# Kernel optimization log

Measured on AMD Instinct MI355X. Metric: run time of the kernel, lower is better.

Reference implementation:

```python
import jax, jax.numpy as jnp
import numpy as np

B, M, N, D, H = 8, 64, 64, 256, 8

def setup_inputs() -> dict:
    key = jax.random.key(0)
    kx, kq, kk, kv, ko = jax.random.split(key, 5)
    x = jax.random.normal(kx, (B, M, N, D), dtype=jnp.float32)
    q = jax.random.normal(kq, (H, D, D), dtype=jnp.float32)
    k = jax.random.normal(kk, (D, D), dtype=jnp.float32)
    v = jax.random.normal(kv, (D, D), dtype=jnp.float32)
    o = jax.random.normal(ko, (H, D, D), dtype=jnp.float32)
    return {"x": x, "q": q, "k": k, "v": v, "o": o}

def reference(x, q, k, v, o):
    # x: [b,m,n,d]; q,o: [h,d,d]; k,v: [d,d]
    Q = jnp.einsum('bmnd,hdk->bhmnk', x, q)      # [b,h,m,n,d]
    h_half = Q.shape[1] // 2
    Q1, Q2 = Q[:, :h_half], Q[:, h_half:]
    K = jnp.einsum('bmnd,dk->bmnk', x, k)        # [b,m,n,d]
    V = jnp.einsum('bmnd,dv->bmnv', x, v)        # [b,m,n,d]

    # Axis 1: attend along the m (row) axis for each column y
    logits1 = jnp.einsum('bhxyk,bzyk->bhyxz', Q1, K)   # [b,h/2,n,m,m]
    scores1 = jax.nn.softmax(logits1, axis=-1)
    O1 = jnp.einsum('bhyxz,bzyv->bhxyv', scores1, V)   # [b,h/2,m,n,d]

    # Axis 2: attend along the n (column) axis for each row x
    logits2 = jnp.einsum('bhxyk,bxzk->bhxyz', Q2, K)   # [b,h/2,m,n,n]
    scores2 = jax.nn.softmax(logits2, axis=-1)
    O2 = jnp.einsum('bhxyz,bxzv->bhxyv', scores2, V)   # [b,h/2,m,n,d]

    O = jnp.concatenate([O1, O2], axis=1)              # [b,h,m,n,d]
    # Faithful to original: 'bhmnd,hdv->bmnd' keeps d, sums over h and v
    Z = jnp.einsum('bhmnd,hdv->bmnd', O, o)
    return Z
```

## Files before the change

### kernel.cpp

```cpp
#include <hip/hip_runtime.h>

typedef unsigned short u16;
typedef __attribute__((ext_vector_type(8))) short short8;
typedef __attribute__((ext_vector_type(4))) float f32x4;

__device__ __forceinline__ float bf2f(u16 u){ return __uint_as_float(((unsigned)u)<<16); }
__device__ __forceinline__ u16 f2bf(float f){
  unsigned u = __float_as_uint(f);
  unsigned r = u + 0x7fffu + ((u>>16)&1u);
  return (u16)(r>>16);
}

#define MFMA16(a,b,c) __builtin_amdgcn_mfma_f32_16x16x32_bf16(a,b,c,0,0,0)

static constexpr int XS_STR  = 264;
static constexpr int PS_STR  = 72;
static constexpr int WT_STR  = 72;
static constexpr int XHI_OFF = 0;
static constexpr int XLO_OFF = 16896;
static constexpr int GT_OFF  = 33792;
static constexpr int XVT_OFF = 50688;
static constexpr int PS_OFF  = 69120;
static constexpr int SMRE_OFF= 73728;
static constexpr int SMEM_BYTES = (73728 + 512)*2;

static constexpr int MH_SMEM = 70656*2;


__global__ void prep_kernel(const float* __restrict__ k, const float* __restrict__ v,
                            const float* __restrict__ o, u16* __restrict__ khi,
                            u16* __restrict__ klo, u16* __restrict__ vT,
                            float* __restrict__ soP, float4* __restrict__ outz){
  __shared__ float Ts[64*65];
  const int blk = blockIdx.x, tid = threadIdx.x;
  if (blk < 64){
    int base = blk*1024 + tid*4;
    const float4 f4 = *(const float4*)(k + base);
    ushort4 hv, lv;
    hv.x=f2bf(f4.x); lv.x=f2bf(f4.x-bf2f(hv.x));
    hv.y=f2bf(f4.y); lv.y=f2bf(f4.y-bf2f(hv.y));
    hv.z=f2bf(f4.z); lv.z=f2bf(f4.z-bf2f(hv.z));
    hv.w=f2bf(f4.w); lv.w=f2bf(f4.w-bf2f(hv.w));
    *(ushort4*)&khi[base] = hv;
    *(ushort4*)&klo[base] = lv;
  } else if (blk < 80){
    int t = blk - 64;
    const int bi = (t>>2)<<6, bj = (t&3)<<6;
    #pragma unroll
    for (int p=0;p<4;p++){
      int idx4 = tid + (p<<8);
      int i = idx4 >> 4, c4 = (idx4 & 15) << 2;
      const float4 f4 = *(const float4*)(v + ((bi+i)<<8) + bj + c4);
      Ts[i*65+c4]=f4.x; Ts[i*65+c4+1]=f4.y; Ts[i*65+c4+2]=f4.z; Ts[i*65+c4+3]=f4.w;
    }
    __syncthreads();
    #pragma unroll
    for (int p=0;p<2;p++){
      int ch = tid + (p<<8);
      int j = ch >> 3, i8 = (ch & 7) << 3;
      short8 t8;
      #pragma unroll
      for (int e=0;e<8;e++) t8[e] = (short)f2bf(Ts[(i8+e)*65 + j]);
      *(short8*)&vT[((bj+j)<<8) + bi + i8] = t8;
    }
  } else if (blk < 336){
    int p = blk - 80;
    int h = p >> 5, base = (p & 31) << 3;
    int w = tid >> 6, l = tid & 63;
    #pragma unroll
    for (int i=0;i<2;i++){
      int row = base + w*2 + i;
      const float4 f4 = *(const float4*)(o + (((h<<8)+row)<<8) + (l<<2));
      float s = f4.x + f4.y + f4.z + f4.w;
      #pragma unroll
      for (int off=32; off>=1; off>>=1) s += __shfl_xor(s, off, 64);
      if (l==0) soP[(h<<8)+row] = s;
    }
  } else {
    int z = blk - 336;
    const float4 zf4 = {0.f,0.f,0.f,0.f};
    #pragma unroll
    for (int i=0;i<16;i++) outz[z*4096 + i*256 + tid] = zf4;
  }
}

__global__ __launch_bounds__(256,1) void mh_kernel(
    const float* __restrict__ q, const u16* __restrict__ khi,
    const u16* __restrict__ klo, u16* __restrict__ mhi, u16* __restrict__ mlo)
{
  extern __shared__ u16 sm[];
  u16* Qhi = sm;
  u16* Qlo = sm + 16896;
  u16* Chi = sm + 33792;
  u16* Clo = sm + 52224;

  const int tid = threadIdx.x;
  const int w = tid >> 6, lane = tid & 63;
  const int quad = lane >> 4, m16 = lane & 15;
  const int cw = w << 6, koq = quad << 3;
  const int h = blockIdx.x >> 2, dt = (blockIdx.x & 3) << 6;

  #pragma unroll
  for (int i=0;i<16;i++){
    int idx4 = i*256 + tid;
    int tr = idx4 >> 6, c4 = (idx4 & 63) << 2;
    const float4 xv = *(const float4*)(q + (((h<<8)+dt+tr)<<8) + c4);
    ushort4 hv, lv;
    hv.x=f2bf(xv.x); lv.x=f2bf(xv.x-bf2f(hv.x));
    hv.y=f2bf(xv.y); lv.y=f2bf(xv.y-bf2f(hv.y));
    hv.z=f2bf(xv.z); lv.z=f2bf(xv.z-bf2f(hv.z));
    hv.w=f2bf(xv.w); lv.w=f2bf(xv.w-bf2f(hv.w));
    *(ushort4*)&Qhi[tr*XS_STR + c4] = hv;
    *(ushort4*)&Qlo[tr*XS_STR + c4] = lv;
  }
  __syncthreads();

  const f32x4 zf = {0.f,0.f,0.f,0.f};
  f32x4 acc[4][4];
  #pragma unroll
  for (int r=0;r<4;r++)
    #pragma unroll
    for (int c=0;c<4;c++) acc[r][c] = zf;

  short8 Bh[2][4], Bl[2][4];
  #pragma unroll
  for (int c=0;c<4;c++){
    Bh[0][c] = *(const short8*)&khi[(cw + c*16 + m16)*256 + koq];
    Bl[0][c] = *(const short8*)&klo[(cw + c*16 + m16)*256 + koq];
  }
  #pragma unroll
  for (int kk=0;kk<8;kk++){
    const int cur = kk&1, nxt = cur^1;
    if (kk<7){
      const int ko2 = ((kk+1)<<5) + koq;
      #pragma unroll
      for (int c=0;c<4;c++){
        Bh[nxt][c] = *(const short8*)&khi[(cw + c*16 + m16)*256 + ko2];
        Bl[nxt][c] = *(const short8*)&klo[(cw + c*16 + m16)*256 + ko2];
      }
    }
    const int ko = (kk<<5) + koq;
    short8 Ah[4], Al[4];
    #pragma unroll
    for (int r=0;r<4;r++) Ah[r] = *(const short8*)&Qhi[(r*16+m16)*XS_STR + ko];
    #pragma unroll
    for (int r=0;r<4;r++) Al[r] = *(const short8*)&Qlo[(r*16+m16)*XS_STR + ko];
    #pragma unroll
    for (int r=0;r<4;r++)
      #pragma unroll
      for (int c=0;c<4;c++){
        acc[r][c] = MFMA16(Ah[r], Bh[cur][c], acc[r][c]);
        acc[r][c] = MFMA16(Ah[r], Bl[cur][c], acc[r][c]);
        acc[r][c] = MFMA16(Al[r], Bh[cur][c], acc[r][c]);
      }
  }

  #pragma unroll
  for (int r=0;r<4;r++)
    #pragma unroll
    for (int c=0;c<4;c++)
      #pragma unroll
      for (int g=0; g<4; g++){
        int drow = r*16 + quad*4 + g;
        int dp   = cw + c*16 + m16;
        float vv = acc[r][c][g];
        u16 hh = f2bf(vv);
        Chi[dp*WT_STR + drow] = hh;
        Clo[dp*WT_STR + drow] = f2bf(vv - bf2f(hh));
      }
  __syncthreads();

  #pragma unroll
  for (int p=0;p<8;p++){
    int ch = tid + (p<<8);
    int dp = ch >> 3, i8 = (ch & 7) << 3;
    *(int4*)&mhi[(((h<<8)+dp)<<8) + dt + i8] = *(const int4*)&Chi[dp*WT_STR + i8];
    *(int4*)&mlo[(((h<<8)+dp)<<8) + dt + i8] = *(const int4*)&Clo[dp*WT_STR + i8];
  }
}

__global__ __launch_bounds__(512,2) void attn_kernel(
    const float* __restrict__ x, const u16* __restrict__ mhiP,
    const u16* __restrict__ mloP, const u16* __restrict__ vT,
    const float* __restrict__ soP, float* __restrict__ out)
{
  extern __shared__ u16 sm[];
  u16* Xhi = sm + XHI_OFF;
  u16* Xlo = sm + XLO_OFF;
  u16* Gt  = sm + GT_OFF;
  u16* Xvt = sm + XVT_OFF;
  u16* Ps  = sm + PS_OFF;
  float* SMf = (float*)(sm + SMRE_OFF);

  const int tid  = threadIdx.x;
  const int w    = tid >> 6, lane = tid & 63;
  const int quad = lane >> 4, m16 = lane & 15;
  const int br   = blockIdx.x >> 9;
  const int idx  = blockIdx.x & 511;
  const int b    = idx >> 6, s = idx & 63;
  const int cw   = w << 5;
  const int rs   = (w >> 1) << 4;
  const int zh   = w & 1;
  const int koq  = quad << 3;

  auto tok = [&](int t)->int {
    int m = br ? s : t;
    int n = br ? t : s;
    return (((b<<6) + m) << 14) + (n << 8);
  };

  #pragma unroll
  for (int i=0;i<8;i++){
    int idx4 = i*512 + tid;
    int tr = idx4 >> 6, c4 = (idx4 & 63) << 2;
    const float4 xv = *(const float4*)(x + tok(tr) + c4);
    ushort4 hv, lv;
    hv.x=f2bf(xv.x); lv.x=f2bf(xv.x-bf2f(hv.x));
    hv.y=f2bf(xv.y); lv.y=f2bf(xv.y-bf2f(hv.y));
    hv.z=f2bf(xv.z); lv.z=f2bf(xv.z-bf2f(hv.z));
    hv.w=f2bf(xv.w); lv.w=f2bf(xv.w-bf2f(hv.w));
    *(ushort4*)&Xhi[tr*XS_STR + c4] = hv;
    *(ushort4*)&Xlo[tr*XS_STR + c4] = lv;
  }
  __syncthreads();

  short8 XB[16];
  #pragma unroll
  for (int kk=0;kk<8;kk++)
    #pragma unroll
    for (int c=0;c<2;c++)
      XB[kk*2+c] = *(const short8*)&Xhi[((zh<<5) + c*16 + m16)*XS_STR + (kk<<5) + koq];

  const f32x4 zf = {0.f,0.f,0.f,0.f};
  f32x4 acc[4][2];

  auto mm3 = [&](const u16* __restrict__ Whi, const u16* __restrict__ Wlo){
    #pragma unroll
    for (int r=0;r<4;r++){ acc[r][0] = zf; acc[r][1] = zf; }
    short8 Bh[2][2], Bl[2][2];
    #pragma unroll
    for (int c=0;c<2;c++){
      Bh[0][c] = *(const short8*)&Whi[(cw + c*16 + m16)*256 + koq];
      Bl[0][c] = *(const short8*)&Wlo[(cw + c*16 + m16)*256 + koq];
    }
    #pragma unroll
    for (int kk=0;kk<8;kk++){
      const int cur = kk&1, nxt = cur^1;
      if (kk<7){
        const int ko2 = ((kk+1)<<5) + koq;
        #pragma unroll
        for (int c=0;c<2;c++){
          Bh[nxt][c] = *(const short8*)&Whi[(cw + c*16 + m16)*256 + ko2];
          Bl[nxt][c] = *(const short8*)&Wlo[(cw + c*16 + m16)*256 + ko2];
        }
      }
      const int ko = (kk<<5) + koq;
      short8 Ah[4], Al[4];
      #pragma unroll
      for (int r=0;r<4;r++) Ah[r] = *(const short8*)&Xhi[(r*16+m16)*XS_STR + ko];
      #pragma unroll
      for (int r=0;r<4;r++) Al[r] = *(const short8*)&Xlo[(r*16+m16)*XS_STR + ko];
      #pragma unroll
      for (int r=0;r<4;r++)
        #pragma unroll
        for (int c=0;c<2;c++){
          acc[r][c] = MFMA16(Ah[r], Bh[cur][c], acc[r][c]);
          acc[r][c] = MFMA16(Ah[r], Bl[cur][c], acc[r][c]);
          acc[r][c] = MFMA16(Al[r], Bh[cur][c], acc[r][c]);
        }
    }
  };

  {
    #pragma unroll
    for (int r=0;r<4;r++){ acc[r][0] = zf; acc[r][1] = zf; }
    #pragma unroll
    for (int kk=0;kk<8;kk++){
      const int ko = (kk<<5) + koq;
      short8 A[4], Bf[2];
      #pragma unroll
      for (int r=0;r<4;r++) A[r]  = *(const short8*)&Xhi[(r*16+m16)*XS_STR + ko];
      #pragma unroll
      for (int c=0;c<2;c++) Bf[c] = *(const short8*)&vT[(cw + c*16 + m16)*256 + ko];
      #pragma unroll
      for (int r=0;r<4;r++)
        #pragma unroll
        for (int c=0;c<2;c++) acc[r][c] = MFMA16(A[r], Bf[c], acc[r][c]);
    }
    #pragma unroll
    for (int r=0;r<4;r++)
      #pragma unroll
      for (int c=0;c<2;c++)
        #pragma unroll
        for (int g=0; g<4; g++){
          int z  = r*16 + quad*4 + g;
          int vc = cw + c*16 + m16;
          Xvt[vc*WT_STR + z] = f2bf(acc[r][c][g]);
        }
  }

  f32x4 Z[4][2];
  #pragma unroll
  for (int r=0;r<4;r++){ Z[r][0] = zf; Z[r][1] = zf; }

  for (int h=0; h<4; h++){
    const int gh = br*4 + h;

    mm3(mhiP + gh*65536, mloP + gh*65536);
    #pragma unroll
    for (int r=0;r<4;r++)
      #pragma unroll
      for (int c=0;c<2;c++)
        #pragma unroll
        for (int g=0; g<4; g++){
          int row = r*16 + quad*4 + g;
          int col = cw + c*16 + m16;
          Gt[row*XS_STR + col] = f2bf(acc[r][c][g]);
        }
    __syncthreads();

    f32x4 L[2];
    L[0] = zf; L[1] = zf;
    #pragma unroll
    for (int kk=0;kk<8;kk++){
      const int ko = (kk<<5) + koq;
      short8 A = *(const short8*)&Gt[(rs+m16)*XS_STR + ko];
      #pragma unroll
      for (int c=0;c<2;c++){
        L[c] = MFMA16(A, XB[kk*2+c], L[c]);
        short8 Bl = *(const short8*)&Xlo[((zh<<5) + c*16 + m16)*XS_STR + ko];
        L[c] = MFMA16(A, Bl, L[c]);
      }
    }
    __syncthreads();
    #pragma unroll
    for (int r=0;r<4;r++)
      #pragma unroll
      for (int c=0;c<2;c++)
        #pragma unroll
        for (int g=0; g<4; g++){
          int row = r*16 + quad*4 + g;
          int col = cw + c*16 + m16;
          float vv = acc[r][c][g];
          u16 hh = f2bf(vv);
          Gt[row*XS_STR + col] = f2bf(vv - bf2f(hh));
        }
    __syncthreads();

    #pragma unroll
    for (int kk=0;kk<8;kk++){
      const int ko = (kk<<5) + koq;
      short8 A = *(const short8*)&Gt[(rs+m16)*XS_STR + ko];
      #pragma unroll
      for (int c=0;c<2;c++)
        L[c] = MFMA16(A, XB[kk*2+c], L[c]);
    }

    float mxl[4], sml[4];
    #pragma unroll
    for (int g=0; g<4; g++){
      float mx = fmaxf(L[0][g], L[1][g]);
      #pragma unroll
      for (int off=1; off<16; off<<=1) mx = fmaxf(mx, __shfl_xor(mx, off, 64));
      float sum = 0.f;
      #pragma unroll
      for (int c=0;c<2;c++){ float e = __expf(L[c][g]-mx); L[c][g] = e; sum += e; }
      #pragma unroll
      for (int off=1; off<16; off<<=1) sum += __shfl_xor(sum, off, 64);
      mxl[g] = mx; sml[g] = sum;
      if (m16 == 0){
        int row = rs + quad*4 + g;
        SMf[row*4 + zh*2]     = mx;
        SMf[row*4 + zh*2 + 1] = sum;
      }
    }
    __syncthreads();
    #pragma unroll
    for (int g=0; g<4; g++){
      int row = rs + quad*4 + g;
      float mxo = SMf[row*4 + (zh^1)*2];
      float smo = SMf[row*4 + (zh^1)*2 + 1];
      float M   = fmaxf(mxl[g], mxo);
      float al  = __expf(mxl[g]-M), ao = __expf(mxo-M);
      float scale = al / (sml[g]*al + smo*ao);
      #pragma unroll
      for (int c=0;c<2;c++)
        Ps[row*PS_STR + (zh<<5) + c*16 + m16] = f2bf(L[c][g]*scale);
    }
    __syncthreads();

    #pragma unroll
    for (int r=0;r<4;r++){ acc[r][0] = zf; acc[r][1] = zf; }
    #pragma unroll
    for (int kk=0;kk<2;kk++){
      const int ko = (kk<<5) + koq;
      short8 A[4], Bf[2];
      #pragma unroll
      for (int r=0;r<4;r++) A[r]  = *(const short8*)&Ps[(r*16+m16)*PS_STR + ko];
      #pragma unroll
      for (int c=0;c<2;c++) Bf[c] = *(const short8*)&Xvt[(cw + c*16 + m16)*WT_STR + ko];
      #pragma unroll
      for (int r=0;r<4;r++)
        #pragma unroll
        for (int c=0;c<2;c++) acc[r][c] = MFMA16(A[r], Bf[c], acc[r][c]);
    }
    float sc[2];
    sc[0] = soP[gh*256 + cw + m16];
    sc[1] = soP[gh*256 + cw + 16 + m16];
    #pragma unroll
    for (int r=0;r<4;r++)
      #pragma unroll
      for (int c=0;c<2;c++)
        #pragma unroll
        for (int g=0; g<4; g++) Z[r][c][g] += sc[c]*acc[r][c][g];
  }

  #pragma unroll
  for (int r=0;r<4;r++)
    #pragma unroll
    for (int c=0;c<2;c++)
      #pragma unroll
      for (int g=0; g<4; g++){
        int t   = r*16 + quad*4 + g;
        int col = cw + c*16 + m16;
        atomicAdd(&out[tok(t) + col], Z[r][c][g]);
      }
}

extern "C" void kernel_launch(void* const* d_in, const int* in_sizes, int n_in,
                              void* d_out, int out_size, void* d_ws, size_t ws_size,
                              hipStream_t stream) {
  const float* x = (const float*)d_in[0];
  const float* q = (const float*)d_in[1];
  const float* k = (const float*)d_in[2];
  const float* v = (const float*)d_in[3];
  const float* o = (const float*)d_in[4];
  u16* ws   = (u16*)d_ws;
  u16* mhi  = ws;
  u16* mlo  = ws + 524288;
  u16* khi  = ws + 1048576;
  u16* klo  = ws + 1114112;
  u16* vT   = ws + 1179648;
  float* soP = (float*)(ws + 1245184);
  float* out = (float*)d_out;

  prep_kernel<<<848, 256, 0, stream>>>(k, v, o, khi, klo, vT, soP, (float4*)d_out);
  (void)hipFuncSetAttribute(reinterpret_cast<const void*>(&mh_kernel),
                            hipFuncAttributeMaxDynamicSharedMemorySize, MH_SMEM);
  mh_kernel<<<32, 256, MH_SMEM, stream>>>(q, khi, klo, mhi, mlo);

  (void)hipFuncSetAttribute(reinterpret_cast<const void*>(&attn_kernel),
                            hipFuncAttributeMaxDynamicSharedMemorySize, SMEM_BYTES);
  attn_kernel<<<1024, 512, SMEM_BYTES, stream>>>(x, mhi, mlo, vT, soP, out);
}
```

Measured before the change: 340.2 us.

## Double attention block to 1024 threads with 2x4 warp tiling and split G hi/lo buffers

Each attention block now runs 16 waves instead of 8. Each wave owns a 32x32 output tile, so per-wave accumulator and register pressure drop. G is stored as separate hi and lo buffers written at once, which removes one barrier round and the second pass over G. The softmax is now reduced across four column quarters instead of two. The V tile is hoisted into registers, and Xvt aliases the G region to fit shared memory. Occupancy per CU may fall to one block because of the shared-memory size, and the 1024-thread launch bound may force register spills.

After: 705.6 us. +107.4%, slower.

```diff
diff --git a/kernel.cpp b/kernel.cpp
--- a/kernel.cpp
+++ b/kernel.cpp
@@ -18,11 +18,12 @@
 static constexpr int WT_STR  = 72;
 static constexpr int XHI_OFF = 0;
 static constexpr int XLO_OFF = 16896;
-static constexpr int GT_OFF  = 33792;
-static constexpr int XVT_OFF = 50688;
-static constexpr int PS_OFF  = 69120;
-static constexpr int SMRE_OFF= 73728;
-static constexpr int SMEM_BYTES = (73728 + 512)*2;
+static constexpr int GHI_OFF = 33792;
+static constexpr int GLO_OFF = 50688;
+static constexpr int XVT_OFF = 33792;
+static constexpr int PS_OFF  = 67584;
+static constexpr int SMF_OFF = 72192;
+static constexpr int SMEM_BYTES = (72192 + 1024)*2;
 
 static constexpr int MH_SMEM = 70656*2;
 
@@ -179,7 +180,7 @@
   }
 }
 
-__global__ __launch_bounds__(512,2) void attn_kernel(
+__global__ __launch_bounds__(1024,4) void attn_kernel(
     const float* __restrict__ x, const u16* __restrict__ mhiP,
     const u16* __restrict__ mloP, const u16* __restrict__ vT,
     const float* __restrict__ soP, float* __restrict__ out)
@@ -187,10 +188,11 @@
   extern __shared__ u16 sm[];
   u16* Xhi = sm + XHI_OFF;
   u16* Xlo = sm + XLO_OFF;
-  u16* Gt  = sm + GT_OFF;
+  u16* Ghi = sm + GHI_OFF;
+  u16* Glo = sm + GLO_OFF;
   u16* Xvt = sm + XVT_OFF;
+  float* SMf = (float*)(sm + SMF_OFF);
   u16* Ps  = sm + PS_OFF;
-  float* SMf = (float*)(sm + SMRE_OFF);
 
   const int tid  = threadIdx.x;
   const int w    = tid >> 6, lane = tid & 63;
@@ -198,9 +200,10 @@
   const int br   = blockIdx.x >> 9;
   const int idx  = blockIdx.x & 511;
   const int b    = idx >> 6, s = idx & 63;
-  const int cw   = w << 5;
-  const int rs   = (w >> 1) << 4;
-  const int zh   = w & 1;
+  const int rb   = (w >> 3) << 5;
+  const int cb   = (w & 7) << 5;
+  const int rs   = (w >> 2) << 4;
+  const int zq   = w & 3;
   const int koq  = quad << 3;
 
   auto tok = [&](int t)->int {
@@ -210,8 +213,8 @@
   };
 
   #pragma unroll
-  for (int i=0;i<8;i++){
-    int idx4 = i*512 + tid;
+  for (int i=0;i<4;i++){
+    int idx4 = i*1024 + tid;
     int tr = idx4 >> 6, c4 = (idx4 & 63) << 2;
     const float4 xv = *(const float4*)(x + tok(tr) + c4);
     ushort4 hv, lv;
@@ -224,191 +227,163 @@
   }
   __syncthreads();
 
-  short8 XB[16];
+  short8 XB[8];
   #pragma unroll
   for (int kk=0;kk<8;kk++)
-    #pragma unroll
-    for (int c=0;c<2;c++)
-      XB[kk*2+c] = *(const short8*)&Xhi[((zh<<5) + c*16 + m16)*XS_STR + (kk<<5) + koq];
+    XB[kk] = *(const short8*)&Xhi[((zq<<4) + m16)*XS_STR + (kk<<5) + koq];
 
   const f32x4 zf = {0.f,0.f,0.f,0.f};
-  f32x4 acc[4][2];
-
-  auto mm3 = [&](const u16* __restrict__ Whi, const u16* __restrict__ Wlo){
-    #pragma unroll
-    for (int r=0;r<4;r++){ acc[r][0] = zf; acc[r][1] = zf; }
-    short8 Bh[2][2], Bl[2][2];
-    #pragma unroll
-    for (int c=0;c<2;c++){
-      Bh[0][c] = *(const short8*)&Whi[(cw + c*16 + m16)*256 + koq];
-      Bl[0][c] = *(const short8*)&Wlo[(cw + c*16 + m16)*256 + koq];
-    }
-    #pragma unroll
-    for (int kk=0;kk<8;kk++){
-      const int cur = kk&1, nxt = cur^1;
-      if (kk<7){
-        const int ko2 = ((kk+1)<<5) + koq;
-        #pragma unroll
-        for (int c=0;c<2;c++){
-          Bh[nxt][c] = *(const short8*)&Whi[(cw + c*16 + m16)*256 + ko2];
-          Bl[nxt][c] = *(const short8*)&Wlo[(cw + c*16 + m16)*256 + ko2];
-        }
-      }
-      const int ko = (kk<<5) + koq;
-      short8 Ah[4], Al[4];
-      #pragma unroll
-      for (int r=0;r<4;r++) Ah[r] = *(const short8*)&Xhi[(r*16+m16)*XS_STR + ko];
-      #pragma unroll
-      for (int r=0;r<4;r++) Al[r] = *(const short8*)&Xlo[(r*16+m16)*XS_STR + ko];
-      #pragma unroll
-      for (int r=0;r<4;r++)
-        #pragma unroll
-        for (int c=0;c<2;c++){
-          acc[r][c] = MFMA16(Ah[r], Bh[cur][c], acc[r][c]);
-          acc[r][c] = MFMA16(Ah[r], Bl[cur][c], acc[r][c]);
-          acc[r][c] = MFMA16(Al[r], Bh[cur][c], acc[r][c]);
-        }
-    }
-  };
+  f32x4 acc[2][2];
 
   {
     #pragma unroll
-    for (int r=0;r<4;r++){ acc[r][0] = zf; acc[r][1] = zf; }
+    for (int r=0;r<2;r++){ acc[r][0] = zf; acc[r][1] = zf; }
     #pragma unroll
     for (int kk=0;kk<8;kk++){
       const int ko = (kk<<5) + koq;
-      short8 A[4], Bf[2];
-      #pragma unroll
-      for (int r=0;r<4;r++) A[r]  = *(const short8*)&Xhi[(r*16+m16)*XS_STR + ko];
-      #pragma unroll
-      for (int c=0;c<2;c++) Bf[c] = *(const short8*)&vT[(cw + c*16 + m16)*256 + ko];
-      #pragma unroll
-      for (int r=0;r<4;r++)
+      short8 A[2], Bf[2];
+      #pragma unroll
+      for (int r=0;r<2;r++) A[r]  = *(const short8*)&Xhi[(rb + r*16 + m16)*XS_STR + ko];
+      #pragma unroll
+      for (int c=0;c<2;c++) Bf[c] = *(const short8*)&vT[(cb + c*16 + m16)*256 + ko];
+      #pragma unroll
+      for (int r=0;r<2;r++)
         #pragma unroll
         for (int c=0;c<2;c++) acc[r][c] = MFMA16(A[r], Bf[c], acc[r][c]);
     }
     #pragma unroll
-    for (int r=0;r<4;r++)
+    for (int r=0;r<2;r++)
       #pragma unroll
       for (int c=0;c<2;c++)
         #pragma unroll
         for (int g=0; g<4; g++){
-          int z  = r*16 + quad*4 + g;
-          int vc = cw + c*16 + m16;
+          int z  = rb + r*16 + quad*4 + g;
+          int vc = cb + c*16 + m16;
           Xvt[vc*WT_STR + z] = f2bf(acc[r][c][g]);
         }
   }
-
-  f32x4 Z[4][2];
-  #pragma unroll
-  for (int r=0;r<4;r++){ Z[r][0] = zf; Z[r][1] = zf; }
+  __syncthreads();
+
+  short8 XvB[2][2];
+  #pragma unroll
+  for (int kk=0;kk<2;kk++)
+    #pragma unroll
+    for (int c=0;c<2;c++)
+      XvB[kk][c] = *(const short8*)&Xvt[(cb + c*16 + m16)*WT_STR + (kk<<5) + koq];
+  __syncthreads();
+
+  f32x4 Z[2][2];
+  #pragma unroll
+  for (int r=0;r<2;r++){ Z[r][0] = zf; Z[r][1] = zf; }
 
   for (int h=0; h<4; h++){
     const int gh = br*4 + h;
-
-    mm3(mhiP + gh*65536, mloP + gh*65536);
-    #pragma unroll
-    for (int r=0;r<4;r++)
+    const u16* __restrict__ Whi = mhiP + gh*65536;
+    const u16* __restrict__ Wlo = mloP + gh*65536;
+
+    #pragma unroll
+    for (int r=0;r<2;r++){ acc[r][0] = zf; acc[r][1] = zf; }
+    #pragma unroll
+    for (int kk=0;kk<8;kk++){
+      const int ko = (kk<<5) + koq;
+      short8 Ah[2], Al[2], Bh[2], Bl[2];
+      #pragma unroll
+      for (int r=0;r<2;r++){
+        Ah[r] = *(const short8*)&Xhi[(rb + r*16 + m16)*XS_STR + ko];
+        Al[r] = *(const short8*)&Xlo[(rb + r*16 + m16)*XS_STR + ko];
+      }
+      #pragma unroll
+      for (int c=0;c<2;c++){
+        Bh[c] = *(const short8*)&Whi[(cb + c*16 + m16)*256 + ko];
+        Bl[c] = *(const short8*)&Wlo[(cb + c*16 + m16)*256 + ko];
+      }
+      #pragma unroll
+      for (int r=0;r<2;r++)
+        #pragma unroll
+        for (int c=0;c<2;c++){
+          acc[r][c] = MFMA16(Ah[r], Bh[c], acc[r][c]);
+          acc[r][c] = MFMA16(Ah[r], Bl[c], acc[r][c]);
+          acc[r][c] = MFMA16(Al[r], Bh[c], acc[r][c]);
+        }
+    }
+    #pragma unroll
+    for (int r=0;r<2;r++)
       #pragma unroll
       for (int c=0;c<2;c++)
         #pragma unroll
         for (int g=0; g<4; g++){
-          int row = r*16 + quad*4 + g;
-          int col = cw + c*16 + m16;
-          Gt[row*XS_STR + col] = f2bf(acc[r][c][g]);
+          int row = rb + r*16 + quad*4 + g;
+          int col = cb + c*16 + m16;
+          float vv = acc[r][c][g];
+          u16 hh = f2bf(vv);
+          Ghi[row*XS_STR + col] = hh;
+          Glo[row*XS_STR + col] = f2bf(vv - bf2f(hh));
         }
     __syncthreads();
 
-    f32x4 L[2];
-    L[0] = zf; L[1] = zf;
+    f32x4 L = zf;
     #pragma unroll
     for (int kk=0;kk<8;kk++){
       const int ko = (kk<<5) + koq;
-      short8 A = *(const short8*)&Gt[(rs+m16)*XS_STR + ko];
-      #pragma unroll
-      for (int c=0;c<2;c++){
-        L[c] = MFMA16(A, XB[kk*2+c], L[c]);
-        short8 Bl = *(const short8*)&Xlo[((zh<<5) + c*16 + m16)*XS_STR + ko];
-        L[c] = MFMA16(A, Bl, L[c]);
-      }
-    }
-    __syncthreads();
-    #pragma unroll
-    for (int r=0;r<4;r++)
-      #pragma unroll
-      for (int c=0;c<2;c++)
-        #pragma unroll
-        for (int g=0; g<4; g++){
-          int row = r*16 + quad*4 + g;
-          int col = cw + c*16 + m16;
-          float vv = acc[r][c][g];
-          u16 hh = f2bf(vv);
-          Gt[row*XS_STR + col] = f2bf(vv - bf2f(hh));
-        }
-    __syncthreads();
-
-    #pragma unroll
-    for (int kk=0;kk<8;kk++){
-      const int ko = (kk<<5) + koq;
-      short8 A = *(const short8*)&Gt[(rs+m16)*XS_STR + ko];
-      #pragma unroll
-      for (int c=0;c<2;c++)
-        L[c] = MFMA16(A, XB[kk*2+c], L[c]);
+      short8 Ahi = *(const short8*)&Ghi[(rs + m16)*XS_STR + ko];
+      short8 Alo = *(const short8*)&Glo[(rs + m16)*XS_STR + ko];
+      short8 Bxl = *(const short8*)&Xlo[((zq<<4) + m16)*XS_STR + ko];
+      L = MFMA16(Ahi, XB[kk], L);
+      L = MFMA16(Ahi, Bxl, L);
+      L = MFMA16(Alo, XB[kk], L);
     }
 
     float mxl[4], sml[4];
     #pragma unroll
     for (int g=0; g<4; g++){
-      float mx = fmaxf(L[0][g], L[1][g]);
+      float mx = L[g];
       #pragma unroll
       for (int off=1; off<16; off<<=1) mx = fmaxf(mx, __shfl_xor(mx, off, 64));
-      float sum = 0.f;
-      #pragma unroll
-      for (int c=0;c<2;c++){ float e = __expf(L[c][g]-mx); L[c][g] = e; sum += e; }
+      float e = __expf(L[g]-mx); L[g] = e;
+      float sum = e;
       #pragma unroll
       for (int off=1; off<16; off<<=1) sum += __shfl_xor(sum, off, 64);
       mxl[g] = mx; sml[g] = sum;
       if (m16 == 0){
         int row = rs + quad*4 + g;
-        SMf[row*4 + zh*2]     = mx;
-        SMf[row*4 + zh*2 + 1] = sum;
+        SMf[row*8 + zq*2]     = mx;
+        SMf[row*8 + zq*2 + 1] = sum;
       }
     }
     __syncthreads();
     #pragma unroll
     for (int g=0; g<4; g++){
       int row = rs + quad*4 + g;
-      float mxo = SMf[row*4 + (zh^1)*2];
-      float smo = SMf[row*4 + (zh^1)*2 + 1];
-      float M   = fmaxf(mxl[g], mxo);
-      float al  = __expf(mxl[g]-M), ao = __expf(mxo-M);
-      float scale = al / (sml[g]*al + smo*ao);
-      #pragma unroll
-      for (int c=0;c<2;c++)
-        Ps[row*PS_STR + (zh<<5) + c*16 + m16] = f2bf(L[c][g]*scale);
+      float m0=SMf[row*8+0], s0=SMf[row*8+1];
+      float m1=SMf[row*8+2], s1=SMf[row*8+3];
+      float m2=SMf[row*8+4], s2=SMf[row*8+5];
+      float m3=SMf[row*8+6], s3=SMf[row*8+7];
+      float M  = fmaxf(fmaxf(m0,m1), fmaxf(m2,m3));
+      float denom = s0*__expf(m0-M) + s1*__expf(m1-M)
+                  + s2*__expf(m2-M) + s3*__expf(m3-M);
+      float scale = __expf(mxl[g]-M)/denom;
+      Ps[row*PS_STR + (zq<<4) + m16] = f2bf(L[g]*scale);
     }
     __syncthreads();
 
     #pragma unroll
-    for (int r=0;r<4;r++){ acc[r][0] = zf; acc[r][1] = zf; }
+    for (int r=0;r<2;r++){ acc[r][0] = zf; acc[r][1] = zf; }
     #pragma unroll
     for (int kk=0;kk<2;kk++){
       const int ko = (kk<<5) + koq;
-      short8 A[4], Bf[2];
-      #pragma unroll
-      for (int r=0;r<4;r++) A[r]  = *(const short8*)&Ps[(r*16+m16)*PS_STR + ko];
-      #pragma unroll
-      for (int c=0;c<2;c++) Bf[c] = *(const short8*)&Xvt[(cw + c*16 + m16)*WT_STR + ko];
-      #pragma unroll
-      for (int r=0;r<4;r++)
-        #pragma unroll
-        for (int c=0;c<2;c++) acc[r][c] = MFMA16(A[r], Bf[c], acc[r][c]);
+      short8 Ap[2];
+      #pragma unroll
+      for (int r=0;r<2;r++) Ap[r] = *(const short8*)&Ps[(rb + r*16 + m16)*PS_STR + ko];
+      #pragma unroll
+      for (int r=0;r<2;r++)
+        #pragma unroll
+        for (int c=0;c<2;c++) acc[r][c] = MFMA16(Ap[r], XvB[kk][c], acc[r][c]);
     }
     float sc[2];
-    sc[0] = soP[gh*256 + cw + m16];
-    sc[1] = soP[gh*256 + cw + 16 + m16];
-    #pragma unroll
-    for (int r=0;r<4;r++)
+    sc[0] = soP[gh*256 + cb + m16];
+    sc[1] = soP[gh*256 + cb + 16 + m16];
+    #pragma unroll
+    for (int r=0;r<2;r++)
       #pragma unroll
       for (int c=0;c<2;c++)
         #pragma unroll
@@ -416,13 +391,13 @@
   }
 
   #pragma unroll
-  for (int r=0;r<4;r++)
+  for (int r=0;r<2;r++)
     #pragma unroll
     for (int c=0;c<2;c++)
       #pragma unroll
       for (int g=0; g<4; g++){
-        int t   = r*16 + quad*4 + g;
-        int col = cw + c*16 + m16;
+        int t   = rb + r*16 + quad*4 + g;
+        int col = cb + c*16 + m16;
         atomicAdd(&out[tok(t) + col], Z[r][c][g]);
       }
 }
@@ -451,5 +426,5 @@
 
   (void)hipFuncSetAttribute(reinterpret_cast<const void*>(&attn_kernel),
                             hipFuncAttributeMaxDynamicSharedMemorySize, SMEM_BYTES);
-  attn_kernel<<<1024, 512, SMEM_BYTES, stream>>>(x, mhi, mlo, vT, soP, out);
+  attn_kernel<<<1024, 1024, SMEM_BYTES, stream>>>(x, mhi, mlo, vT, soP, out);
 }
```

## Split mh_kernel into smaller tiles across 256 blocks for more parallelism

Applied to the files above, without the earlier changes.

The q·k weight-precombination kernel now launches 256 blocks, each computing a 32x64 output tile instead of a 64x256 tile, so only 32 of the many CUs are no longer the only ones busy. Per-block shared memory and register use shrink, and the k operand is loaded directly without double buffering. The cost is more redundant loading of q rows and k columns across blocks and less MFMA work per wave to hide latency.

Result: no change. 335.5 us (-1.4%).

```diff
diff --git a/kernel.cpp b/kernel.cpp
--- a/kernel.cpp
+++ b/kernel.cpp
@@ -24,7 +24,7 @@
 static constexpr int SMRE_OFF= 73728;
 static constexpr int SMEM_BYTES = (73728 + 512)*2;
 
-static constexpr int MH_SMEM = 70656*2;
+static constexpr int MH_SMEM = 22016*2;
 
 
 __global__ void prep_kernel(const float* __restrict__ k, const float* __restrict__ v,
@@ -90,18 +90,21 @@
 {
   extern __shared__ u16 sm[];
   u16* Qhi = sm;
-  u16* Qlo = sm + 16896;
-  u16* Chi = sm + 33792;
-  u16* Clo = sm + 52224;
+  u16* Qlo = sm + 8448;
+  u16* Chi = sm + 16896;
+  u16* Clo = sm + 19456;
 
   const int tid = threadIdx.x;
   const int w = tid >> 6, lane = tid & 63;
   const int quad = lane >> 4, m16 = lane & 15;
-  const int cw = w << 6, koq = quad << 3;
-  const int h = blockIdx.x >> 2, dt = (blockIdx.x & 3) << 6;
-
-  #pragma unroll
-  for (int i=0;i<16;i++){
+  const int cw2 = w << 4, koq = quad << 3;
+  const int h   = blockIdx.x >> 5;
+  const int rr  = blockIdx.x & 31;
+  const int dt  = (rr >> 2) << 5;
+  const int dpq = (rr & 3) << 6;
+
+  #pragma unroll
+  for (int i=0;i<8;i++){
     int idx4 = i*256 + tid;
     int tr = idx4 >> 6, c4 = (idx4 & 63) << 2;
     const float4 xv = *(const float4*)(q + (((h<<8)+dt+tr)<<8) + c4);
@@ -116,67 +119,35 @@
   __syncthreads();
 
   const f32x4 zf = {0.f,0.f,0.f,0.f};
-  f32x4 acc[4][4];
-  #pragma unroll
-  for (int r=0;r<4;r++)
-    #pragma unroll
-    for (int c=0;c<4;c++) acc[r][c] = zf;
-
-  short8 Bh[2][4], Bl[2][4];
-  #pragma unroll
-  for (int c=0;c<4;c++){
-    Bh[0][c] = *(const short8*)&khi[(cw + c*16 + m16)*256 + koq];
-    Bl[0][c] = *(const short8*)&klo[(cw + c*16 + m16)*256 + koq];
-  }
+  f32x4 a0 = zf, a1 = zf;
   #pragma unroll
   for (int kk=0;kk<8;kk++){
-    const int cur = kk&1, nxt = cur^1;
-    if (kk<7){
-      const int ko2 = ((kk+1)<<5) + koq;
-      #pragma unroll
-      for (int c=0;c<4;c++){
-        Bh[nxt][c] = *(const short8*)&khi[(cw + c*16 + m16)*256 + ko2];
-        Bl[nxt][c] = *(const short8*)&klo[(cw + c*16 + m16)*256 + ko2];
-      }
-    }
     const int ko = (kk<<5) + koq;
-    short8 Ah[4], Al[4];
-    #pragma unroll
-    for (int r=0;r<4;r++) Ah[r] = *(const short8*)&Qhi[(r*16+m16)*XS_STR + ko];
-    #pragma unroll
-    for (int r=0;r<4;r++) Al[r] = *(const short8*)&Qlo[(r*16+m16)*XS_STR + ko];
-    #pragma unroll
-    for (int r=0;r<4;r++)
-      #pragma unroll
-      for (int c=0;c<4;c++){
-        acc[r][c] = MFMA16(Ah[r], Bh[cur][c], acc[r][c]);
-        acc[r][c] = MFMA16(Ah[r], Bl[cur][c], acc[r][c]);
-        acc[r][c] = MFMA16(Al[r], Bh[cur][c], acc[r][c]);
-      }
-  }
-
-  #pragma unroll
-  for (int r=0;r<4;r++)
-    #pragma unroll
-    for (int c=0;c<4;c++)
-      #pragma unroll
-      for (int g=0; g<4; g++){
-        int drow = r*16 + quad*4 + g;
-        int dp   = cw + c*16 + m16;
-        float vv = acc[r][c][g];
-        u16 hh = f2bf(vv);
-        Chi[dp*WT_STR + drow] = hh;
-        Clo[dp*WT_STR + drow] = f2bf(vv - bf2f(hh));
-      }
+    short8 Ah0 = *(const short8*)&Qhi[(m16)*XS_STR + ko];
+    short8 Al0 = *(const short8*)&Qlo[(m16)*XS_STR + ko];
+    short8 Ah1 = *(const short8*)&Qhi[(16+m16)*XS_STR + ko];
+    short8 Al1 = *(const short8*)&Qlo[(16+m16)*XS_STR + ko];
+    short8 Bh  = *(const short8*)&khi[(dpq+cw2+m16)*256 + ko];
+    short8 Bl  = *(const short8*)&klo[(dpq+cw2+m16)*256 + ko];
+    a0 = MFMA16(Ah0,Bh,a0); a0 = MFMA16(Ah0,Bl,a0); a0 = MFMA16(Al0,Bh,a0);
+    a1 = MFMA16(Ah1,Bh,a1); a1 = MFMA16(Ah1,Bl,a1); a1 = MFMA16(Al1,Bh,a1);
+  }
+
+  const int dpl = cw2 + m16;
+  #pragma unroll
+  for (int g=0; g<4; g++){
+    float v0 = a0[g]; u16 h0 = f2bf(v0);
+    Chi[dpl*40 + quad*4+g] = h0;
+    Clo[dpl*40 + quad*4+g] = f2bf(v0 - bf2f(h0));
+    float v1 = a1[g]; u16 h1 = f2bf(v1);
+    Chi[dpl*40 + 16 + quad*4+g] = h1;
+    Clo[dpl*40 + 16 + quad*4+g] = f2bf(v1 - bf2f(h1));
+  }
   __syncthreads();
 
-  #pragma unroll
-  for (int p=0;p<8;p++){
-    int ch = tid + (p<<8);
-    int dp = ch >> 3, i8 = (ch & 7) << 3;
-    *(int4*)&mhi[(((h<<8)+dp)<<8) + dt + i8] = *(const int4*)&Chi[dp*WT_STR + i8];
-    *(int4*)&mlo[(((h<<8)+dp)<<8) + dt + i8] = *(const int4*)&Clo[dp*WT_STR + i8];
-  }
+  int dpo = tid >> 2, i8 = (tid & 3) << 3;
+  *(int4*)&mhi[(((h<<8)+dpq+dpo)<<8) + dt + i8] = *(const int4*)&Chi[dpo*40 + i8];
+  *(int4*)&mlo[(((h<<8)+dpq+dpo)<<8) + dt + i8] = *(const int4*)&Clo[dpo*40 + i8];
 }
 
 __global__ __launch_bounds__(512,2) void attn_kernel(
@@ -447,7 +418,7 @@
   prep_kernel<<<848, 256, 0, stream>>>(k, v, o, khi, klo, vT, soP, (float4*)d_out);
   (void)hipFuncSetAttribute(reinterpret_cast<const void*>(&mh_kernel),
                             hipFuncAttributeMaxDynamicSharedMemorySize, MH_SMEM);
-  mh_kernel<<<32, 256, MH_SMEM, stream>>>(q, khi, klo, mhi, mlo);
+  mh_kernel<<<256, 256, MH_SMEM, stream>>>(q, khi, klo, mhi, mlo);
 
   (void)hipFuncSetAttribute(reinterpret_cast<const void*>(&attn_kernel),
                             hipFuncAttributeMaxDynamicSharedMemorySize, SMEM_BYTES);
```
